# Kernel optimization log

Measured on AMD Instinct MI355X. Metric: run time of the kernel, lower is better.

Reference implementation:

```python
import jax, jax.numpy as jnp
import numpy as np

B, N, F, NCG, NCONV, VOCAB = 16, 1024, 128, 64, 3, 100
EPS = 0.001


def setup_inputs() -> dict:
    key = jax.random.key(0)
    ks = jax.random.split(key, 16)
    atoms_nodes = jax.random.randint(ks[0], (B, N), 0, VOCAB, dtype=jnp.int32)
    xyz = jax.random.normal(ks[1], (B, N, 3), jnp.float32) * 3.0
    # chain bonds (i, i+1) per molecule -> every atom has degree >= 1
    bi = jnp.repeat(jnp.arange(B), N - 1)
    si = jnp.tile(jnp.arange(N - 1), B)
    bonds = jnp.stack([bi, si, si + 1], axis=1).astype(jnp.int32)  # [B*(N-1), 3]
    tau = jnp.float32(1.0)
    gumbel_u = jax.random.uniform(ks[2], (B, N, NCG), jnp.float32, 1e-6, 1.0 - 1e-6)
    # parameters
    emb = jax.random.normal(ks[3], (VOCAB, F), jnp.float32) * 0.1
    emb = emb.at[0].set(0.0)  # padding_idx=0
    s = 1.0 / np.sqrt(F)
    upd_W1 = jax.random.uniform(ks[4], (NCONV, F, F), jnp.float32, -s, s)
    upd_b1 = jax.random.uniform(ks[5], (NCONV, F), jnp.float32, -s, s)
    upd_W2 = jax.random.uniform(ks[6], (NCONV, F, F), jnp.float32, -s, s)
    upd_b2 = jax.random.uniform(ks[7], (NCONV, F), jnp.float32, -s, s)
    cg_W1 = jax.random.uniform(ks[8], (F, F), jnp.float32, -s, s)
    cg_b1 = jax.random.uniform(ks[9], (F,), jnp.float32, -s, s)
    cg_W2 = jax.random.uniform(ks[10], (F, NCG), jnp.float32, -s, s)
    cg_b2 = jax.random.uniform(ks[11], (NCG,), jnp.float32, -s, s)
    return {"atoms_nodes": atoms_nodes, "xyz": xyz, "bonds": bonds, "tau": tau,
            "gumbel_u": gumbel_u, "emb": emb,
            "upd_W1": upd_W1, "upd_b1": upd_b1, "upd_W2": upd_W2, "upd_b2": upd_b2,
            "cg_W1": cg_W1, "cg_b1": cg_b1, "cg_W2": cg_W2, "cg_b2": cg_b2}


def reference(atoms_nodes, xyz, bonds, tau, gumbel_u, emb,
              upd_W1, upd_b1, upd_W2, upd_b2, cg_W1, cg_b1, cg_W2, cg_b2):
    h = emb[atoms_nodes]  # [B,N,F]
    # dense symmetric adjacency from bond list
    adj = jnp.zeros((B, N, N), jnp.float32)
    adj = adj.at[bonds[:, 0], bonds[:, 1], bonds[:, 2]].set(1.0)
    adj = adj.at[bonds[:, 0], bonds[:, 2], bonds[:, 1]].set(1.0)
    deg = jnp.sum(adj, axis=-1)[:, :, None]  # [B,N,1]
    for l in range(NCONV):
        ch = jnp.tanh(h @ upd_W1[l] + upd_b1[l]) @ upd_W2[l] + upd_b2[l]
        dh = jnp.einsum('bif,bij->bjf', ch, adj) / deg
        h = h + dh
    # gumbel-softmax assignment (soft)
    assign_logits = jnp.tanh(h @ cg_W1 + cg_b1) @ cg_W2 + cg_b2  # [B,N,NCG]
    g = -jnp.log(-jnp.log(gumbel_u))
    M = jax.nn.softmax((assign_logits + g) / tau, axis=-1)  # [B,N,NCG]
    M_norm = M / jnp.sum(M, axis=-2, keepdims=True)
    H = jnp.einsum('bnj,bnf->bjf', M_norm, h)        # [B,NCG,F]
    cg_xyz = jnp.einsum('bin,bij->bjn', xyz, M_norm)  # [B,NCG,3]
    cg_adj = jnp.broadcast_to(jnp.ones((NCG, NCG)) - jnp.eye(NCG), (B, NCG, NCG))
    diff = cg_xyz[:, :, None, :] - cg_xyz[:, None, :, :]
    dist = jnp.sqrt(jnp.sum(diff * diff, axis=-1) + EPS)  # [B,NCG,NCG]
    knbrs = jnp.argsort(dist, axis=-1)
    return (M, M_norm, h, H, adj, cg_xyz, cg_adj, knbrs)
```

## Files before the change

kernel.cpp:

```cpp
#include <hip/hip_runtime.h>
#include <hip/hip_bf16.h>
#include <math.h>

#define BB 16
#define NN 1024
#define FF 128
#define NCG 64
#define NCONV 3
#define CAP 8

static const size_t O_M     = 0;
static const size_t O_MN    = (size_t)BB*NN*NCG;
static const size_t O_H     = O_MN  + (size_t)BB*NN*NCG;
static const size_t O_HH    = O_H   + (size_t)BB*NN*FF;
static const size_t O_ADJ   = O_HH  + (size_t)BB*NCG*FF;
static const size_t O_CGXYZ = O_ADJ + (size_t)BB*NN*NN;
static const size_t O_CGADJ = O_CGXYZ + (size_t)BB*NCG*3;
static const size_t O_KN    = O_CGADJ + (size_t)BB*NCG*NCG;

static const size_t S_H64  = 0;
static const size_t S_T64  = (size_t)BB*NN*FF;
static const size_t S_LM64 = S_T64 + (size_t)BB*NN*FF;
static const size_t S_HP   = S_LM64 + (size_t)BB*NN*NCG;
static const size_t S_CGP  = S_HP + 8*(size_t)BB*NCG*FF;
static const size_t S_NBR  = S_CGP + 8*(size_t)BB*NCG*3;

static const size_t W_INVD = 0;
static const size_t W_COLS = (size_t)BB*NN;
static const size_t W_CG64 = W_COLS + (size_t)BB*NCG;
static const size_t W_CNT  = W_CG64 + (size_t)BB*NCG*3;

__global__ void k_zero(int* cnt, double* colsum) {
    int i = blockIdx.x * blockDim.x + threadIdx.x;
    if (i < BB*NN) cnt[i] = 0;
    if (i < BB*NCG) colsum[i] = 0.0;
}

__global__ void k_build_nbr(const int* __restrict__ bonds, int nb, int* cnt, int* nbr) {
    int i = blockIdx.x * blockDim.x + threadIdx.x;
    if (i >= nb) return;
    int b = bonds[i*3+0], s = bonds[i*3+1], t = bonds[i*3+2];
    int ns = b*NN + s, nt = b*NN + t;
    int p = atomicAdd(&cnt[ns], 1);
    if (p < CAP) nbr[(size_t)ns*CAP + p] = nt;
    int q = atomicAdd(&cnt[nt], 1);
    if (q < CAP) nbr[(size_t)nt*CAP + q] = ns;
}

__global__ void k_invdeg(const int* __restrict__ cnt, double* invdeg) {
    int i = blockIdx.x * blockDim.x + threadIdx.x;
    if (i >= BB*NN) return;
    int d = cnt[i];
    invdeg[i] = d > 0 ? 1.0 / (double)d : 0.0;
}

__global__ void k_cgadj(float* cgadj) {
    int idx = blockIdx.x * blockDim.x + threadIdx.x;
    if (idx >= BB*NCG*NCG) return;
    int i = (idx / NCG) % NCG, j = idx % NCG;
    cgadj[idx] = (i == j) ? 0.f : 1.f;
}

__global__ void k_emb64(const int* __restrict__ atoms, const float* __restrict__ emb,
                        double* __restrict__ h) {
    int idx = blockIdx.x * blockDim.x + threadIdx.x;
    if (idx >= BB*NN*(FF/4)) return;
    int n = idx / (FF/4), f4 = idx % (FF/4);
    int a = atoms[n];
    const float4 v = *reinterpret_cast<const float4*>(&emb[(size_t)a*FF + f4*4]);
    double* hp = &h[(size_t)n*FF + f4*4];
    hp[0] = (double)v.x; hp[1] = (double)v.y; hp[2] = (double)v.z; hp[3] = (double)v.w;
}

template<int COUT, bool TANH>
__global__ __launch_bounds__(256) void k_gemm64(const double* __restrict__ in,
                                                const float* __restrict__ W,
                                                const float* __restrict__ bias,
                                                double* __restrict__ out) {
    constexpr int K = 128, ROWS = 64, KC = 32;
    constexpr int ASTR = KC + 2;
    constexpr int CT = COUT / 8;
    constexpr int RT = 256 / CT;
    constexpr int RPT = ROWS / RT;
    constexpr int GS = COUT / 4;
    __shared__ double As[ROWS * ASTR];
    __shared__ double Ws[KC * COUT];
    const int tid = threadIdx.x;
    const size_t row0 = (size_t)blockIdx.x * ROWS;
    const int tc = tid % CT, tr = tid / CT;
    const int r0 = tr * RPT;

    double acc[RPT][8];
    #pragma unroll
    for (int i = 0; i < RPT; ++i)
        #pragma unroll
        for (int j = 0; j < 8; ++j) acc[i][j] = 0.0;

    const double2* in2 = reinterpret_cast<const double2*>(in + row0 * K);

    for (int kc = 0; kc < K; kc += KC) {
        __syncthreads();
        #pragma unroll
        for (int i = 0; i < 4; ++i) {
            int q = tid + i*256;
            int row = q >> 4, c2 = q & 15;
            *reinterpret_cast<double2*>(&As[row*ASTR + c2*2]) = in2[row*64 + (kc>>1) + c2];
        }
        {
            const float4* Wg = reinterpret_cast<const float4*>(W + (size_t)kc * COUT);
            #pragma unroll
            for (int i = 0; i < KC*COUT/4/256; ++i) {
                int q = tid + i*256;
                float4 w = Wg[q];
                Ws[q*4+0] = (double)w.x; Ws[q*4+1] = (double)w.y;
                Ws[q*4+2] = (double)w.z; Ws[q*4+3] = (double)w.w;
            }
        }
        __syncthreads();
        #pragma unroll
        for (int kk = 0; kk < KC; ++kk) {
            double a_[RPT];
            #pragma unroll
            for (int i = 0; i < RPT; ++i) a_[i] = As[(r0+i)*ASTR + kk];
            const double2* wb = reinterpret_cast<const double2*>(&Ws[kk*COUT]);
            double2 wg[4];
            #pragma unroll
            for (int g = 0; g < 4; ++g) wg[g] = wb[tc + g*CT];
            #pragma unroll
            for (int i = 0; i < RPT; ++i)
                #pragma unroll
                for (int g = 0; g < 4; ++g) {
                    acc[i][g*2+0] += a_[i] * wg[g].x;
                    acc[i][g*2+1] += a_[i] * wg[g].y;
                }
        }
    }

    double bv[8];
    #pragma unroll
    for (int g = 0; g < 4; ++g) {
        bv[g*2+0] = (double)bias[tc*2 + g*GS + 0];
        bv[g*2+1] = (double)bias[tc*2 + g*GS + 1];
    }
    #pragma unroll
    for (int i = 0; i < RPT; ++i) {
        double2* op = reinterpret_cast<double2*>(out + (row0 + r0 + i) * COUT);
        #pragma unroll
        for (int g = 0; g < 4; ++g) {
            double v0 = acc[i][g*2+0] + bv[g*2+0];
            double v1 = acc[i][g*2+1] + bv[g*2+1];
            if (TANH) { v0 = tanh(v0); v1 = tanh(v1); }
            double2 o; o.x = v0; o.y = v1;
            op[tc + g*CT] = o;
        }
    }
}

template<bool WRITE_F32>
__global__ void k_gather(const double* __restrict__ ch, const double* __restrict__ invdeg,
                         const int* __restrict__ nbr, const int* __restrict__ cnt,
                         double* __restrict__ h, float* __restrict__ hout) {
    int idx = blockIdx.x * blockDim.x + threadIdx.x;
    if (idx >= BB*NN*(FF/4)) return;
    int node = idx >> 5, f4 = idx & 31;
    int c = cnt[node];
    double2 s0; s0.x = 0.0; s0.y = 0.0;
    double2 s1 = s0;
    for (int q = 0; q < c; ++q) {
        int nb = nbr[(size_t)node*CAP + q];
        const double2* cp = reinterpret_cast<const double2*>(ch + (size_t)nb*FF + f4*4);
        double2 a = cp[0], b2 = cp[1];
        s0.x += a.x; s0.y += a.y; s1.x += b2.x; s1.y += b2.y;
    }
    double w = invdeg[node];
    double2* hp = reinterpret_cast<double2*>(h + (size_t)node*FF + f4*4);
    double2 h0 = hp[0], h1 = hp[1];
    h0.x += s0.x*w; h0.y += s0.y*w; h1.x += s1.x*w; h1.y += s1.y*w;
    hp[0] = h0; hp[1] = h1;
    if (WRITE_F32) {
        float4 o; o.x = (float)h0.x; o.y = (float)h0.y; o.z = (float)h1.x; o.w = (float)h1.y;
        *reinterpret_cast<float4*>(&hout[(size_t)node*FF + f4*4]) = o;
    }
}

__global__ void k_softmax64(double* __restrict__ lm, const float* __restrict__ gum,
                            const float* __restrict__ tau_p, float* __restrict__ M_out,
                            double* __restrict__ colsum) {
    int row = blockIdx.x * 4 + threadIdx.x / 64;
    int lane = threadIdx.x & 63;
    double tau = (double)(*tau_p);
    double u = (double)gum[(size_t)row*NCG + lane];
    double g = -log(-log(u));
    double v = (lm[(size_t)row*NCG + lane] + g) / tau;
    double m = v;
    #pragma unroll
    for (int off = 32; off; off >>= 1) m = fmax(m, __shfl_xor(m, off));
    double e = exp(v - m);
    double s = e;
    #pragma unroll
    for (int off = 32; off; off >>= 1) s += __shfl_xor(s, off);
    double mv = e / s;
    lm[(size_t)row*NCG + lane] = mv;
    M_out[(size_t)row*NCG + lane] = (float)mv;
    atomicAdd(&colsum[(row >> 10) * NCG + lane], mv);
}

__global__ void k_mnorm_out(const double* __restrict__ M, const double* __restrict__ colsum,
                            float* __restrict__ Mn) {
    size_t i = (size_t)blockIdx.x * blockDim.x + threadIdx.x;
    if (i >= (size_t)BB*NN*NCG) return;
    size_t b = i >> 16;
    int j = (int)(i & 63);
    Mn[i] = (float)(M[i] / colsum[b*NCG + j]);
}

__global__ __launch_bounds__(256) void k_Hpart(const double* __restrict__ M,
                                               const double* __restrict__ h,
                                               double* __restrict__ Hp) {
    __shared__ double Ms[32*NCG];
    __shared__ double hs[32*FF];
    const int b = blockIdx.x, ch = blockIdx.y;
    const int tid = threadIdx.x;
    const int tc = tid % 32, tr = tid / 32;
    const double2* M2 = reinterpret_cast<const double2*>(M + (size_t)b*NN*NCG);
    const double2* h2 = reinterpret_cast<const double2*>(h + (size_t)b*NN*FF);
    double2* Ms2 = reinterpret_cast<double2*>(Ms);
    double2* hs2 = reinterpret_cast<double2*>(hs);

    double acc[8][4];
    #pragma unroll
    for (int i = 0; i < 8; ++i)
        #pragma unroll
        for (int j = 0; j < 4; ++j) acc[i][j] = 0.0;

    for (int s = 0; s < 4; ++s) {
        const int n0 = ch*128 + s*32;
        __syncthreads();
        #pragma unroll
        for (int i = 0; i < 4; ++i) Ms2[tid + i*256] = M2[n0*32 + tid + i*256];
        #pragma unroll
        for (int i = 0; i < 8; ++i) hs2[tid + i*256] = h2[n0*64 + tid + i*256];
        __syncthreads();
        for (int n = 0; n < 32; ++n) {
            double2 hv0 = hs2[n*64 + tc];
            double2 hv1 = hs2[n*64 + 32 + tc];
            double2 m0 = Ms2[n*32 + tr];
            double2 m1 = Ms2[n*32 + 8 + tr];
            double2 m2 = Ms2[n*32 + 16 + tr];
            double2 m3 = Ms2[n*32 + 24 + tr];
            double mj[8] = {m0.x, m0.y, m1.x, m1.y, m2.x, m2.y, m3.x, m3.y};
            #pragma unroll
            for (int jj = 0; jj < 8; ++jj) {
                acc[jj][0] += mj[jj]*hv0.x; acc[jj][1] += mj[jj]*hv0.y;
                acc[jj][2] += mj[jj]*hv1.x; acc[jj][3] += mj[jj]*hv1.y;
            }
        }
    }
    double* Ho = Hp + ((size_t)ch*BB + b) * NCG * FF;
    #pragma unroll
    for (int gj = 0; gj < 4; ++gj)
        #pragma unroll
        for (int pj = 0; pj < 2; ++pj) {
            int j = tr*2 + gj*16 + pj;
            int jj = gj*2 + pj;
            double2* op = reinterpret_cast<double2*>(Ho + (size_t)j*FF);
            double2 o0; o0.x = acc[jj][0]; o0.y = acc[jj][1];
            double2 o1; o1.x = acc[jj][2]; o1.y = acc[jj][3];
            op[tc] = o0; op[32 + tc] = o1;
        }
}

__global__ void k_Hfin(const double* __restrict__ Hp, const double* __restrict__ colsum,
                       float* __restrict__ H) {
    int idx = blockIdx.x * blockDim.x + threadIdx.x;
    if (idx >= BB*NCG*FF) return;
    int b = idx / (NCG*FF);
    int j = (idx / FF) % NCG;
    double s = 0.0;
    #pragma unroll
    for (int c = 0; c < 8; ++c) s += Hp[((size_t)c*BB + b)*NCG*FF + (idx % (NCG*FF))];
    H[idx] = (float)(s / colsum[b*NCG + j]);
}

__global__ __launch_bounds__(192) void k_cgpart(const double* __restrict__ M,
                                                const float* __restrict__ xyz,
                                                double* __restrict__ cgp) {
    __shared__ double Ms[32*NCG];
    __shared__ double xs[32*3];
    const int b = blockIdx.x, ch = blockIdx.y;
    const int tid = threadIdx.x;
    const int j = tid / 3, d = tid % 3;
    const double2* M2 = reinterpret_cast<const double2*>(M + (size_t)b*NN*NCG);
    double2* Ms2 = reinterpret_cast<double2*>(Ms);
    const float* xb = xyz + (size_t)b*NN*3;
    double acc = 0.0;
    for (int s = 0; s < 4; ++s) {
        const int n0 = ch*128 + s*32;
        __syncthreads();
        for (int q = tid; q < 1024; q += 192) Ms2[q] = M2[n0*32 + q];
        for (int q = tid; q < 96; q += 192) xs[q] = (double)xb[n0*3 + q];
        __syncthreads();
        for (int n = 0; n < 32; ++n)
            acc += Ms[n*NCG + j] * xs[n*3 + d];
    }
    cgp[((size_t)ch*BB + b)*NCG*3 + tid] = acc;
}

__global__ void k_cgfin(const double* __restrict__ cgp, const double* __restrict__ colsum,
                        double* __restrict__ cg64, float* __restrict__ cg) {
    int idx = blockIdx.x * blockDim.x + threadIdx.x;
    if (idx >= BB*NCG*3) return;
    int b = idx / (NCG*3);
    int r = idx % (NCG*3);
    int j = r / 3;
    double s = 0.0;
    #pragma unroll
    for (int c = 0; c < 8; ++c) s += cgp[((size_t)c*BB + b)*NCG*3 + r];
    double v = s / colsum[b*NCG + j];
    cg64[idx] = v;
    cg[idx] = (float)v;
}

__global__ __launch_bounds__(1024) void k_knbrs(const double* __restrict__ cg,
                                                float* __restrict__ kn) {
    __shared__ double cs[NCG*3];
    const int b = blockIdx.x;
    const int tid = threadIdx.x;
    const int i = blockIdx.y * 16 + tid / 64;
    const int j = tid & 63;
    if (tid < NCG*3) cs[tid] = cg[(size_t)b*NCG*3 + tid];
    __syncthreads();
    double xi = cs[i*3+0], yi = cs[i*3+1], zi = cs[i*3+2];
    double dxj = xi - cs[j*3+0], dyj = yi - cs[j*3+1], dzj = zi - cs[j*3+2];
    double d2j = dxj*dxj + dyj*dyj + dzj*dzj;
    int rank = 0;
    for (int k = 0; k < NCG; ++k) {
        double dx = xi - cs[k*3+0], dy = yi - cs[k*3+1], dz = zi - cs[k*3+2];
        double d2k = dx*dx + dy*dy + dz*dz;
        rank += (d2k < d2j) || (d2k == d2j && k < j);
    }
    kn[(size_t)b*NCG*NCG + (size_t)i*NCG + rank] = (float)j;
}

__global__ void k_zero_adj(float4* adj4, long n4) {
    long i = (long)blockIdx.x * blockDim.x + threadIdx.x;
    long stride = (long)gridDim.x * blockDim.x;
    float4 z; z.x = z.y = z.z = z.w = 0.f;
    for (; i < n4; i += stride) adj4[i] = z;
}

__global__ void k_bonds_adj(const int* __restrict__ bonds, int nb, float* adj) {
    int i = blockIdx.x * blockDim.x + threadIdx.x;
    if (i >= nb) return;
    int b = bonds[i*3+0], s = bonds[i*3+1], t = bonds[i*3+2];
    size_t base = (size_t)b * NN * NN;
    adj[base + (size_t)s*NN + t] = 1.f;
    adj[base + (size_t)t*NN + s] = 1.f;
}

extern "C" void kernel_launch(void* const* d_in, const int* in_sizes, int n_in,
                              void* d_out, int out_size, void* d_ws, size_t ws_size,
                              hipStream_t stream) {
    const int*   atoms  = (const int*)  d_in[0];
    const float* xyz    = (const float*)d_in[1];
    const int*   bonds  = (const int*)  d_in[2];
    const float* tau    = (const float*)d_in[3];
    const float* gum    = (const float*)d_in[4];
    const float* emb    = (const float*)d_in[5];
    const float* uW1    = (const float*)d_in[6];
    const float* ub1    = (const float*)d_in[7];
    const float* uW2    = (const float*)d_in[8];
    const float* ub2    = (const float*)d_in[9];
    const float* cgW1   = (const float*)d_in[10];
    const float* cgb1   = (const float*)d_in[11];
    const float* cgW2   = (const float*)d_in[12];
    const float* cgb2   = (const float*)d_in[13];

    float* out = (float*)d_out;
    float* o_M   = out + O_M;
    float* o_Mn  = out + O_MN;
    float* o_h   = out + O_H;
    float* o_H   = out + O_HH;
    float* o_adj = out + O_ADJ;
    float* o_cg  = out + O_CGXYZ;
    float* o_ca  = out + O_CGADJ;
    float* o_kn  = out + O_KN;

    double* scr  = (double*)o_adj;
    double* h64  = scr + S_H64;
    double* t64  = scr + S_T64;
    double* lm64 = scr + S_LM64;
    double* Hp   = scr + S_HP;
    double* cgp  = scr + S_CGP;
    int*    nbr  = (int*)(scr + S_NBR);

    double* wsd    = (double*)d_ws;
    double* invdeg = wsd + W_INVD;
    double* colsum = wsd + W_COLS;
    double* cg64   = wsd + W_CG64;
    int*    cnt    = (int*)(wsd + W_CNT);

    const int nb = in_sizes[2] / 3;

    hipLaunchKernelGGL(k_zero, dim3(64), dim3(256), 0, stream, cnt, colsum);
    hipLaunchKernelGGL(k_build_nbr, dim3((nb+255)/256), dim3(256), 0, stream,
                       bonds, nb, cnt, nbr);
    hipLaunchKernelGGL(k_invdeg, dim3(64), dim3(256), 0, stream, cnt, invdeg);
    hipLaunchKernelGGL(k_cgadj, dim3(256), dim3(256), 0, stream, o_ca);
    hipLaunchKernelGGL(k_emb64, dim3(2048), dim3(256), 0, stream, atoms, emb, h64);

    for (int l = 0; l < NCONV; ++l) {
        hipLaunchKernelGGL((k_gemm64<128,true>), dim3(256), dim3(256), 0, stream,
                           h64, uW1 + (size_t)l*FF*FF, ub1 + (size_t)l*FF, t64);
        hipLaunchKernelGGL((k_gemm64<128,false>), dim3(256), dim3(256), 0, stream,
                           t64, uW2 + (size_t)l*FF*FF, ub2 + (size_t)l*FF, t64);
        if (l < NCONV-1)
            hipLaunchKernelGGL((k_gather<false>), dim3(2048), dim3(256), 0, stream,
                               t64, invdeg, nbr, cnt, h64, o_h);
        else
            hipLaunchKernelGGL((k_gather<true>), dim3(2048), dim3(256), 0, stream,
                               t64, invdeg, nbr, cnt, h64, o_h);
    }

    hipLaunchKernelGGL((k_gemm64<128,true>), dim3(256), dim3(256), 0, stream,
                       h64, cgW1, cgb1, t64);
    hipLaunchKernelGGL((k_gemm64<64,false>), dim3(256), dim3(256), 0, stream,
                       t64, cgW2, cgb2, lm64);

    hipLaunchKernelGGL(k_softmax64, dim3(4096), dim3(256), 0, stream,
                       lm64, gum, tau, o_M, colsum);
    hipLaunchKernelGGL(k_mnorm_out, dim3(4096), dim3(256), 0, stream, lm64, colsum, o_Mn);
    hipLaunchKernelGGL(k_Hpart, dim3(BB, 8), dim3(256), 0, stream, lm64, h64, Hp);
    hipLaunchKernelGGL(k_Hfin, dim3(512), dim3(256), 0, stream, Hp, colsum, o_H);
    hipLaunchKernelGGL(k_cgpart, dim3(BB, 8), dim3(192), 0, stream, lm64, xyz, cgp);
    hipLaunchKernelGGL(k_cgfin, dim3(12), dim3(256), 0, stream, cgp, colsum, cg64, o_cg);
    hipLaunchKernelGGL(k_knbrs, dim3(BB, 4), dim3(1024), 0, stream, cg64, o_kn);

    hipLaunchKernelGGL(k_zero_adj, dim3(4096), dim3(256), 0, stream,
                       (float4*)o_adj, (long)BB*NN*NN/4);
    hipLaunchKernelGGL(k_bonds_adj, dim3((nb+255)/256), dim3(256), 0, stream,
                       bonds, nb, o_adj);
}
```

Measured before the change: 352.7 us.

## Fuse two-layer MLP GEMMs, pre-convert weights to fp64, fp32 H pooling

```diff
diff --git a/kernel.cpp b/kernel.cpp
--- a/kernel.cpp
+++ b/kernel.cpp
@@ -1,5 +1,4 @@
 #include <hip/hip_runtime.h>
-#include <hip/hip_bf16.h>
 #include <math.h>
 
 #define BB 16
@@ -19,21 +18,26 @@
 static const size_t O_KN    = O_CGADJ + (size_t)BB*NCG*NCG;
 
 static const size_t S_H64  = 0;
-static const size_t S_T64  = (size_t)BB*NN*FF;
-static const size_t S_LM64 = S_T64 + (size_t)BB*NN*FF;
-static const size_t S_HP   = S_LM64 + (size_t)BB*NN*NCG;
-static const size_t S_CGP  = S_HP + 8*(size_t)BB*NCG*FF;
-static const size_t S_NBR  = S_CGP + 8*(size_t)BB*NCG*3;
+static const size_t S_CH64 = (size_t)BB*NN*FF;
+static const size_t S_LM64 = S_CH64 + (size_t)BB*NN*FF;
+static const size_t S_HPF  = 5242880;
+static const size_t S_CGP  = 5767168;
+static const size_t S_NBR  = 6291456;
+static const size_t S_W64  = 6553600;
+
+static const size_t WO_CONV = 0;
+static const size_t WO_CGW1 = 98304;
+static const size_t WO_CGW2 = 114688;
+static const int    W64_N   = 122880;
 
 static const size_t W_INVD = 0;
 static const size_t W_COLS = (size_t)BB*NN;
 static const size_t W_CG64 = W_COLS + (size_t)BB*NCG;
 static const size_t W_CNT  = W_CG64 + (size_t)BB*NCG*3;
 
-__global__ void k_zero(int* cnt, double* colsum) {
+__global__ void k_zero(int* cnt) {
     int i = blockIdx.x * blockDim.x + threadIdx.x;
     if (i < BB*NN) cnt[i] = 0;
-    if (i < BB*NCG) colsum[i] = 0.0;
 }
 
 __global__ void k_build_nbr(const int* __restrict__ bonds, int nb, int* cnt, int* nbr) {
@@ -72,86 +76,156 @@
     hp[0] = (double)v.x; hp[1] = (double)v.y; hp[2] = (double)v.z; hp[3] = (double)v.w;
 }
 
-template<int COUT, bool TANH>
-__global__ __launch_bounds__(256) void k_gemm64(const double* __restrict__ in,
-                                                const float* __restrict__ W,
-                                                const float* __restrict__ bias,
-                                                double* __restrict__ out) {
-    constexpr int K = 128, ROWS = 64, KC = 32;
-    constexpr int ASTR = KC + 2;
-    constexpr int CT = COUT / 8;
-    constexpr int RT = 256 / CT;
-    constexpr int RPT = ROWS / RT;
-    constexpr int GS = COUT / 4;
-    __shared__ double As[ROWS * ASTR];
-    __shared__ double Ws[KC * COUT];
+__global__ void k_cvtW(const float* __restrict__ uW1, const float* __restrict__ uW2,
+                       const float* __restrict__ cgW1, const float* __restrict__ cgW2,
+                       double* __restrict__ W64) {
+    int idx = blockIdx.x * blockDim.x + threadIdx.x;
+    if (idx >= W64_N) return;
+    float v;
+    if (idx < 98304) {
+        int l = idx >> 15, r = idx & 32767;
+        v = (r < 16384) ? uW1[l*16384 + r] : uW2[l*16384 + (r & 16383)];
+    } else if (idx < 114688) {
+        v = cgW1[idx - 98304];
+    } else {
+        v = cgW2[idx - 114688];
+    }
+    W64[idx] = (double)v;
+}
+
+template<int COUT2>
+__global__ __launch_bounds__(256) void k_layer(const double* __restrict__ in,
+        const double* __restrict__ W1, const float* __restrict__ b1,
+        const double* __restrict__ W2, const float* __restrict__ b2,
+        double* __restrict__ out) {
+    constexpr int K = 128, KC = 32;
+    constexpr int ASTR = 34, TSTR = 130;
+    constexpr int NW2 = KC*COUT2/2/256;
+    __shared__ double As[32*ASTR];
+    __shared__ double ts[32*TSTR];
+    __shared__ double Ws[KC*128];
     const int tid = threadIdx.x;
-    const size_t row0 = (size_t)blockIdx.x * ROWS;
-    const int tc = tid % CT, tr = tid / CT;
-    const int r0 = tr * RPT;
-
-    double acc[RPT][8];
-    #pragma unroll
-    for (int i = 0; i < RPT; ++i)
+    const size_t row0 = (size_t)blockIdx.x * 32;
+    const double2* in2  = reinterpret_cast<const double2*>(in + row0*K);
+    const double2* W1_2 = reinterpret_cast<const double2*>(W1);
+    const double2* W2_2 = reinterpret_cast<const double2*>(W2);
+    double2* Ws2 = reinterpret_cast<double2*>(Ws);
+
+    const int tc = tid & 15, tr = tid >> 4;
+    const int r0 = tr * 2;
+
+    double acc[2][8];
+    #pragma unroll
+    for (int i = 0; i < 2; ++i)
         #pragma unroll
         for (int j = 0; j < 8; ++j) acc[i][j] = 0.0;
 
-    const double2* in2 = reinterpret_cast<const double2*>(in + row0 * K);
+    double2 pA[2], pW[8];
+    #pragma unroll
+    for (int i = 0; i < 2; ++i) { int q = tid + i*256; pA[i] = in2[(q>>4)*64 + (q&15)]; }
+    #pragma unroll
+    for (int i = 0; i < 8; ++i) pW[i] = W1_2[tid + i*256];
 
     for (int kc = 0; kc < K; kc += KC) {
         __syncthreads();
         #pragma unroll
-        for (int i = 0; i < 4; ++i) {
+        for (int i = 0; i < 2; ++i) {
             int q = tid + i*256;
-            int row = q >> 4, c2 = q & 15;
-            *reinterpret_cast<double2*>(&As[row*ASTR + c2*2]) = in2[row*64 + (kc>>1) + c2];
-        }
-        {
-            const float4* Wg = reinterpret_cast<const float4*>(W + (size_t)kc * COUT);
-            #pragma unroll
-            for (int i = 0; i < KC*COUT/4/256; ++i) {
-                int q = tid + i*256;
-                float4 w = Wg[q];
-                Ws[q*4+0] = (double)w.x; Ws[q*4+1] = (double)w.y;
-                Ws[q*4+2] = (double)w.z; Ws[q*4+3] = (double)w.w;
+            *reinterpret_cast<double2*>(&As[(q>>4)*ASTR + (q&15)*2]) = pA[i];
+        }
+        #pragma unroll
+        for (int i = 0; i < 8; ++i) Ws2[tid + i*256] = pW[i];
+        if (kc + KC < K) {
+            const int kn = kc + KC;
+            #pragma unroll
+            for (int i = 0; i < 2; ++i) { int q = tid + i*256; pA[i] = in2[(q>>4)*64 + (kn>>1) + (q&15)]; }
+            #pragma unroll
+            for (int i = 0; i < 8; ++i) pW[i] = W1_2[kn*64 + tid + i*256];
+        }
+        __syncthreads();
+        #pragma unroll
+        for (int kk2 = 0; kk2 < KC/2; ++kk2) {
+            double2 a0 = *reinterpret_cast<const double2*>(&As[(r0+0)*ASTR + kk2*2]);
+            double2 a1 = *reinterpret_cast<const double2*>(&As[(r0+1)*ASTR + kk2*2]);
+            const double2* w0 = reinterpret_cast<const double2*>(&Ws[(kk2*2+0)*128]);
+            const double2* w1 = reinterpret_cast<const double2*>(&Ws[(kk2*2+1)*128]);
+            #pragma unroll
+            for (int g = 0; g < 4; ++g) {
+                double2 u0 = w0[tc + g*16];
+                double2 u1 = w1[tc + g*16];
+                acc[0][g*2+0] += a0.x*u0.x; acc[0][g*2+1] += a0.x*u0.y;
+                acc[1][g*2+0] += a1.x*u0.x; acc[1][g*2+1] += a1.x*u0.y;
+                acc[0][g*2+0] += a0.y*u1.x; acc[0][g*2+1] += a0.y*u1.y;
+                acc[1][g*2+0] += a1.y*u1.x; acc[1][g*2+1] += a1.y*u1.y;
             }
         }
-        __syncthreads();
-        #pragma unroll
-        for (int kk = 0; kk < KC; ++kk) {
-            double a_[RPT];
-            #pragma unroll
-            for (int i = 0; i < RPT; ++i) a_[i] = As[(r0+i)*ASTR + kk];
-            const double2* wb = reinterpret_cast<const double2*>(&Ws[kk*COUT]);
-            double2 wg[4];
-            #pragma unroll
-            for (int g = 0; g < 4; ++g) wg[g] = wb[tc + g*CT];
-            #pragma unroll
-            for (int i = 0; i < RPT; ++i)
+    }
+    #pragma unroll
+    for (int g = 0; g < 4; ++g) {
+        int c = tc*2 + g*32;
+        double bb0 = (double)b1[c], bb1 = (double)b1[c+1];
+        #pragma unroll
+        for (int i = 0; i < 2; ++i) {
+            double2 o;
+            o.x = tanh(acc[i][g*2+0] + bb0);
+            o.y = tanh(acc[i][g*2+1] + bb1);
+            *reinterpret_cast<double2*>(&ts[(r0+i)*TSTR + c]) = o;
+        }
+    }
+
+    constexpr int CT2  = COUT2/8;
+    constexpr int RPT2 = (COUT2 == 128) ? 2 : 1;
+    const int tc2 = tid % CT2, tr2 = tid / CT2;
+    const int rB = tr2 * RPT2;
+    double acc2[RPT2][8];
+    #pragma unroll
+    for (int i = 0; i < RPT2; ++i)
+        #pragma unroll
+        for (int j = 0; j < 8; ++j) acc2[i][j] = 0.0;
+
+    #pragma unroll
+    for (int i = 0; i < NW2; ++i) pW[i] = W2_2[tid + i*256];
+
+    for (int kc = 0; kc < K; kc += KC) {
+        __syncthreads();
+        #pragma unroll
+        for (int i = 0; i < NW2; ++i) Ws2[tid + i*256] = pW[i];
+        if (kc + KC < K) {
+            const int kn = kc + KC;
+            #pragma unroll
+            for (int i = 0; i < NW2; ++i) pW[i] = W2_2[kn*(COUT2/2) + tid + i*256];
+        }
+        __syncthreads();
+        #pragma unroll
+        for (int kk2 = 0; kk2 < KC/2; ++kk2) {
+            double2 a[RPT2];
+            #pragma unroll
+            for (int i = 0; i < RPT2; ++i)
+                a[i] = *reinterpret_cast<const double2*>(&ts[(rB+i)*TSTR + kc + kk2*2]);
+            const double2* w0 = reinterpret_cast<const double2*>(&Ws[(kk2*2+0)*COUT2]);
+            const double2* w1 = reinterpret_cast<const double2*>(&Ws[(kk2*2+1)*COUT2]);
+            #pragma unroll
+            for (int g = 0; g < 4; ++g) {
+                double2 u0 = w0[tc2 + g*CT2];
+                double2 u1 = w1[tc2 + g*CT2];
                 #pragma unroll
-                for (int g = 0; g < 4; ++g) {
-                    acc[i][g*2+0] += a_[i] * wg[g].x;
-                    acc[i][g*2+1] += a_[i] * wg[g].y;
+                for (int i = 0; i < RPT2; ++i) {
+                    acc2[i][g*2+0] += a[i].x*u0.x; acc2[i][g*2+1] += a[i].x*u0.y;
+                    acc2[i][g*2+0] += a[i].y*u1.x; acc2[i][g*2+1] += a[i].y*u1.y;
                 }
-        }
-    }
-
-    double bv[8];
+            }
+        }
+    }
     #pragma unroll
     for (int g = 0; g < 4; ++g) {
-        bv[g*2+0] = (double)bias[tc*2 + g*GS + 0];
-        bv[g*2+1] = (double)bias[tc*2 + g*GS + 1];
-    }
-    #pragma unroll
-    for (int i = 0; i < RPT; ++i) {
-        double2* op = reinterpret_cast<double2*>(out + (row0 + r0 + i) * COUT);
-        #pragma unroll
-        for (int g = 0; g < 4; ++g) {
-            double v0 = acc[i][g*2+0] + bv[g*2+0];
-            double v1 = acc[i][g*2+1] + bv[g*2+1];
-            if (TANH) { v0 = tanh(v0); v1 = tanh(v1); }
-            double2 o; o.x = v0; o.y = v1;
-            op[tc + g*CT] = o;
+        int c = tc2*2 + g*(COUT2/4);
+        double bb0 = (double)b2[c], bb1 = (double)b2[c+1];
+        #pragma unroll
+        for (int i = 0; i < RPT2; ++i) {
+            double2 o;
+            o.x = acc2[i][g*2+0] + bb0;
+            o.y = acc2[i][g*2+1] + bb1;
+            *reinterpret_cast<double2*>(&out[(row0 + rB + i)*COUT2 + c]) = o;
         }
     }
 }
@@ -184,8 +258,7 @@
 }
 
 __global__ void k_softmax64(double* __restrict__ lm, const float* __restrict__ gum,
-                            const float* __restrict__ tau_p, float* __restrict__ M_out,
-                            double* __restrict__ colsum) {
+                            const float* __restrict__ tau_p, float* __restrict__ M_out) {
     int row = blockIdx.x * 4 + threadIdx.x / 64;
     int lane = threadIdx.x & 63;
     double tau = (double)(*tau_p);
@@ -202,7 +275,22 @@
     double mv = e / s;
     lm[(size_t)row*NCG + lane] = mv;
     M_out[(size_t)row*NCG + lane] = (float)mv;
-    atomicAdd(&colsum[(row >> 10) * NCG + lane], mv);
+}
+
+__global__ __launch_bounds__(256) void k_cols(const double* __restrict__ M,
+                                              double* __restrict__ colsum) {
+    __shared__ double red[256];
+    int b = blockIdx.x;
+    int tid = threadIdx.x;
+    int j = tid & 63, q = tid >> 6;
+    const double* Mb = M + (size_t)b*NN*NCG;
+    double s = 0.0;
+    for (int n = q*256; n < q*256 + 256; ++n) s += Mb[(size_t)n*NCG + j];
+    red[tid] = s;
+    __syncthreads();
+    if (tid < 64) {
+        colsum[b*NCG + j] = red[j] + red[64+j] + red[128+j] + red[192+j];
+    }
 }
 
 __global__ void k_mnorm_out(const double* __restrict__ M, const double* __restrict__ colsum,
@@ -214,41 +302,43 @@
     Mn[i] = (float)(M[i] / colsum[b*NCG + j]);
 }
 
-__global__ __launch_bounds__(256) void k_Hpart(const double* __restrict__ M,
-                                               const double* __restrict__ h,
-                                               double* __restrict__ Hp) {
-    __shared__ double Ms[32*NCG];
-    __shared__ double hs[32*FF];
+__global__ __launch_bounds__(256) void k_Hpart32(const float* __restrict__ Mn,
+                                                 const float* __restrict__ h,
+                                                 float* __restrict__ Hp) {
+    __shared__ float Ms[32*NCG];
+    __shared__ float hs[32*FF];
     const int b = blockIdx.x, ch = blockIdx.y;
     const int tid = threadIdx.x;
     const int tc = tid % 32, tr = tid / 32;
-    const double2* M2 = reinterpret_cast<const double2*>(M + (size_t)b*NN*NCG);
-    const double2* h2 = reinterpret_cast<const double2*>(h + (size_t)b*NN*FF);
-    double2* Ms2 = reinterpret_cast<double2*>(Ms);
-    double2* hs2 = reinterpret_cast<double2*>(hs);
-
-    double acc[8][4];
+    const float4* M4 = reinterpret_cast<const float4*>(Mn + (size_t)b*NN*NCG);
+    const float4* h4 = reinterpret_cast<const float4*>(h + (size_t)b*NN*FF);
+    float4* Ms4 = reinterpret_cast<float4*>(Ms);
+    float4* hs4 = reinterpret_cast<float4*>(hs);
+    const float2* Ms2 = reinterpret_cast<const float2*>(Ms);
+    const float2* hs2 = reinterpret_cast<const float2*>(hs);
+
+    float acc[8][4];
     #pragma unroll
     for (int i = 0; i < 8; ++i)
         #pragma unroll
-        for (int j = 0; j < 4; ++j) acc[i][j] = 0.0;
+        for (int j = 0; j < 4; ++j) acc[i][j] = 0.f;
 
     for (int s = 0; s < 4; ++s) {
         const int n0 = ch*128 + s*32;
         __syncthreads();
         #pragma unroll
-        for (int i = 0; i < 4; ++i) Ms2[tid + i*256] = M2[n0*32 + tid + i*256];
-        #pragma unroll
-        for (int i = 0; i < 8; ++i) hs2[tid + i*256] = h2[n0*64 + tid + i*256];
+        for (int i = 0; i < 2; ++i) Ms4[tid + i*256] = M4[n0*16 + tid + i*256];
+        #pragma unroll
+        for (int i = 0; i < 4; ++i) hs4[tid + i*256] = h4[n0*32 + tid + i*256];
         __syncthreads();
         for (int n = 0; n < 32; ++n) {
-            double2 hv0 = hs2[n*64 + tc];
-            double2 hv1 = hs2[n*64 + 32 + tc];
-            double2 m0 = Ms2[n*32 + tr];
-            double2 m1 = Ms2[n*32 + 8 + tr];
-            double2 m2 = Ms2[n*32 + 16 + tr];
-            double2 m3 = Ms2[n*32 + 24 + tr];
-            double mj[8] = {m0.x, m0.y, m1.x, m1.y, m2.x, m2.y, m3.x, m3.y};
+            float2 hv0 = hs2[n*64 + tc];
+            float2 hv1 = hs2[n*64 + 32 + tc];
+            float2 m0 = Ms2[n*32 + tr];
+            float2 m1 = Ms2[n*32 + 8 + tr];
+            float2 m2 = Ms2[n*32 + 16 + tr];
+            float2 m3 = Ms2[n*32 + 24 + tr];
+            float mj[8] = {m0.x, m0.y, m1.x, m1.y, m2.x, m2.y, m3.x, m3.y};
             #pragma unroll
             for (int jj = 0; jj < 8; ++jj) {
                 acc[jj][0] += mj[jj]*hv0.x; acc[jj][1] += mj[jj]*hv0.y;
@@ -256,30 +346,29 @@
             }
         }
     }
-    double* Ho = Hp + ((size_t)ch*BB + b) * NCG * FF;
+    float* Ho = Hp + ((size_t)ch*BB + b) * NCG * FF;
     #pragma unroll
     for (int gj = 0; gj < 4; ++gj)
         #pragma unroll
         for (int pj = 0; pj < 2; ++pj) {
             int j = tr*2 + gj*16 + pj;
             int jj = gj*2 + pj;
-            double2* op = reinterpret_cast<double2*>(Ho + (size_t)j*FF);
-            double2 o0; o0.x = acc[jj][0]; o0.y = acc[jj][1];
-            double2 o1; o1.x = acc[jj][2]; o1.y = acc[jj][3];
+            float2 o0; o0.x = acc[jj][0]; o0.y = acc[jj][1];
+            float2 o1; o1.x = acc[jj][2]; o1.y = acc[jj][3];
+            float2* op = reinterpret_cast<float2*>(Ho + (size_t)j*FF);
             op[tc] = o0; op[32 + tc] = o1;
         }
 }
 
-__global__ void k_Hfin(const double* __restrict__ Hp, const double* __restrict__ colsum,
-                       float* __restrict__ H) {
+__global__ void k_Hfin32(const float* __restrict__ Hp, float* __restrict__ H) {
     int idx = blockIdx.x * blockDim.x + threadIdx.x;
     if (idx >= BB*NCG*FF) return;
     int b = idx / (NCG*FF);
-    int j = (idx / FF) % NCG;
-    double s = 0.0;
-    #pragma unroll
-    for (int c = 0; c < 8; ++c) s += Hp[((size_t)c*BB + b)*NCG*FF + (idx % (NCG*FF))];
-    H[idx] = (float)(s / colsum[b*NCG + j]);
+    int r = idx % (NCG*FF);
+    float s = 0.f;
+    #pragma unroll
+    for (int c = 0; c < 8; ++c) s += Hp[((size_t)c*BB + b)*NCG*FF + r];
+    H[idx] = s;
 }
 
 __global__ __launch_bounds__(192) void k_cgpart(const double* __restrict__ M,
@@ -388,11 +477,12 @@
 
     double* scr  = (double*)o_adj;
     double* h64  = scr + S_H64;
-    double* t64  = scr + S_T64;
+    double* ch64 = scr + S_CH64;
     double* lm64 = scr + S_LM64;
-    double* Hp   = scr + S_HP;
+    float*  Hpf  = (float*)(scr + S_HPF);
     double* cgp  = scr + S_CGP;
     int*    nbr  = (int*)(scr + S_NBR);
+    double* W64  = scr + S_W64;
 
     double* wsd    = (double*)d_ws;
     double* invdeg = wsd + W_INVD;
@@ -402,36 +492,36 @@
 
     const int nb = in_sizes[2] / 3;
 
-    hipLaunchKernelGGL(k_zero, dim3(64), dim3(256), 0, stream, cnt, colsum);
+    hipLaunchKernelGGL(k_zero, dim3(64), dim3(256), 0, stream, cnt);
     hipLaunchKernelGGL(k_build_nbr, dim3((nb+255)/256), dim3(256), 0, stream,
                        bonds, nb, cnt, nbr);
     hipLaunchKernelGGL(k_invdeg, dim3(64), dim3(256), 0, stream, cnt, invdeg);
     hipLaunchKernelGGL(k_cgadj, dim3(256), dim3(256), 0, stream, o_ca);
+    hipLaunchKernelGGL(k_cvtW, dim3((W64_N+255)/256), dim3(256), 0, stream,
+                       uW1, uW2, cgW1, cgW2, W64);
     hipLaunchKernelGGL(k_emb64, dim3(2048), dim3(256), 0, stream, atoms, emb, h64);
 
     for (int l = 0; l < NCONV; ++l) {
-        hipLaunchKernelGGL((k_gemm64<128,true>), dim3(256), dim3(256), 0, stream,
-                           h64, uW1 + (size_t)l*FF*FF, ub1 + (size_t)l*FF, t64);
-        hipLaunchKernelGGL((k_gemm64<128,false>), dim3(256), dim3(256), 0, stream,
-                           t64, uW2 + (size_t)l*FF*FF, ub2 + (size_t)l*FF, t64);
+        hipLaunchKernelGGL((k_layer<128>), dim3(512), dim3(256), 0, stream,
+                           h64, W64 + (size_t)l*32768, ub1 + (size_t)l*FF,
+                           W64 + (size_t)l*32768 + 16384, ub2 + (size_t)l*FF, ch64);
         if (l < NCONV-1)
             hipLaunchKernelGGL((k_gather<false>), dim3(2048), dim3(256), 0, stream,
-                               t64, invdeg, nbr, cnt, h64, o_h);
+                               ch64, invdeg, nbr, cnt, h64, o_h);
         else
             hipLaunchKernelGGL((k_gather<true>), dim3(2048), dim3(256), 0, stream,
-                               t64, invdeg, nbr, cnt, h64, o_h);
-    }
-
-    hipLaunchKernelGGL((k_gemm64<128,true>), dim3(256), dim3(256), 0, stream,
-                       h64, cgW1, cgb1, t64);
-    hipLaunchKernelGGL((k_gemm64<64,false>), dim3(256), dim3(256), 0, stream,
-                       t64, cgW2, cgb2, lm64);
+                               ch64, invdeg, nbr, cnt, h64, o_h);
+    }
+
+    hipLaunchKernelGGL((k_layer<64>), dim3(512), dim3(256), 0, stream,
+                       h64, W64 + WO_CGW1, cgb1, W64 + WO_CGW2, cgb2, lm64);
 
     hipLaunchKernelGGL(k_softmax64, dim3(4096), dim3(256), 0, stream,
-                       lm64, gum, tau, o_M, colsum);
+                       lm64, gum, tau, o_M);
+    hipLaunchKernelGGL(k_cols, dim3(16), dim3(256), 0, stream, lm64, colsum);
     hipLaunchKernelGGL(k_mnorm_out, dim3(4096), dim3(256), 0, stream, lm64, colsum, o_Mn);
-    hipLaunchKernelGGL(k_Hpart, dim3(BB, 8), dim3(256), 0, stream, lm64, h64, Hp);
-    hipLaunchKernelGGL(k_Hfin, dim3(512), dim3(256), 0, stream, Hp, colsum, o_H);
+    hipLaunchKernelGGL(k_Hpart32, dim3(BB, 8), dim3(256), 0, stream, o_Mn, o_h, Hpf);
+    hipLaunchKernelGGL(k_Hfin32, dim3(512), dim3(256), 0, stream, Hpf, o_H);
     hipLaunchKernelGGL(k_cgpart, dim3(BB, 8), dim3(192), 0, stream, lm64, xyz, cgp);
     hipLaunchKernelGGL(k_cgfin, dim3(12), dim3(256), 0, stream, cgp, colsum, cg64, o_cg);
     hipLaunchKernelGGL(k_knbrs, dim3(BB, 4), dim3(1024), 0, stream, cg64, o_kn);
```

New measurement: 419.8 us. 1.19x slower.
